# Performance work log

Hardware: AMD Instinct MI355X
Metric: run time of the kernel (lower is better)

The kernel has to match this reference:

```python
import jax, jax.numpy as jnp
import numpy as np

B, V, J, K, G, L, E = 8, 262144, 64, 4, 2048, 8, 1835008


def _qmul(q1, q2):
    # quaternion product, (w, x, y, z) convention; broadcasts over leading dims
    w1, v1 = q1[..., :1], q1[..., 1:]
    w2, v2 = q2[..., :1], q2[..., 1:]
    w = w1 * w2 - jnp.sum(v1 * v2, axis=-1, keepdims=True)
    v = w1 * v2 + w2 * v1 + jnp.cross(v1, v2)
    return jnp.concatenate([w, v], axis=-1)


def _qrot(q, v):
    # rotate vector v by unit quaternion q (w, x, y, z)
    qv, qw = q[..., 1:], q[..., :1]
    return v + 2.0 * jnp.cross(qv, jnp.cross(qv, v) + qw * v)


def setup_inputs() -> dict:
    key = jax.random.key(0)
    ks = jax.random.split(key, 13)
    return {
        "temp_verts": jax.random.normal(ks[0], (V, 3), dtype=jnp.float32),
        "joint_quat": jax.random.normal(ks[1], (B, J, 4), dtype=jnp.float32),
        "joint_trans": jax.random.normal(ks[2], (B, J, 3), dtype=jnp.float32),
        "skin_w": jax.random.uniform(ks[3], (V, K), dtype=jnp.float32),
        "node_pos": jax.random.normal(ks[4], (G, 3), dtype=jnp.float32),
        "node_quat": jax.random.normal(ks[5], (B, G, 4), dtype=jnp.float32),
        "node_trans": jax.random.normal(ks[6], (B, G, 3), dtype=jnp.float32),
        "link_w": jax.random.uniform(ks[7], (V, L), dtype=jnp.float32),
        "lap_w": jax.random.normal(ks[8], (E,), dtype=jnp.float32) * 0.1,
        "skin_idx": jax.random.randint(ks[9], (V, K), 0, J),
        "link_idx": jax.random.randint(ks[10], (V, L), 0, G),
        "lap_st": jax.random.randint(ks[11], (E,), 0, V),
        "lap_ed": jax.random.randint(ks[12], (E,), 0, V),
    }


def reference(temp_verts, joint_quat, joint_trans, skin_w, node_pos, node_quat,
              node_trans, link_w, lap_w, skin_idx, link_idx, lap_st, lap_ed):
    eps = 1e-8
    # ----- embedded-graph deformation of the template -----
    lw = link_w / (jnp.sum(link_w, axis=-1, keepdims=True) + eps)      # [V,L]
    nq = node_quat[:, link_idx]                                        # [B,V,L,4]
    nq = nq / (jnp.linalg.norm(nq, axis=-1, keepdims=True) + eps)
    nt = node_trans[:, link_idx]                                       # [B,V,L,3]
    gp = node_pos[link_idx]                                            # [V,L,3]
    local = temp_verts[:, None, :] - gp                                # [V,L,3]
    warped = _qrot(nq, local[None]) + gp[None] + nt                    # [B,V,L,3]
    v_eg = jnp.sum(lw[None, :, :, None] * warped, axis=2)              # [B,V,3]

    # ----- dual-quaternion skinning -----
    jq = joint_quat / (jnp.linalg.norm(joint_quat, axis=-1, keepdims=True) + eps)  # [B,J,4]
    t0 = jnp.concatenate([jnp.zeros_like(joint_trans[..., :1]), joint_trans], axis=-1)
    jd = 0.5 * _qmul(t0, jq)                                           # dual part [B,J,4]

    sw = skin_w / (jnp.sum(skin_w, axis=-1, keepdims=True) + eps)      # [V,K]
    r = jq[:, skin_idx]                                                # [B,V,K,4]
    d = jd[:, skin_idx]                                                # [B,V,K,4]
    # sign-fix against first influence to avoid antipodal blending
    sgn = jnp.where(jnp.sum(r * r[..., :1, :], axis=-1, keepdims=True) >= 0.0, 1.0, -1.0)
    w = sw[None, :, :, None] * sgn                                     # [B,V,K,1]
    rb = jnp.sum(w * r, axis=2)                                        # [B,V,4]
    db = jnp.sum(w * d, axis=2)                                        # [B,V,4]
    nrm = jnp.linalg.norm(rb, axis=-1, keepdims=True) + eps
    rb, db = rb / nrm, db / nrm
    rw, rv = rb[..., :1], rb[..., 1:]
    dw, dv = db[..., :1], db[..., 1:]
    trans = 2.0 * (rw * dv - dw * rv + jnp.cross(rv, dv))              # [B,V,3]
    posed = _qrot(rb, v_eg) + trans                                    # [B,V,3]

    # ----- sparse Laplacian regularization term (COO scatter) -----
    def _lap(p):
        return jax.ops.segment_sum(lap_w[:, None] * p[lap_ed], lap_st, num_segments=V)
    lap = jax.vmap(_lap)(posed)                                        # [B,V,3]

    return jnp.stack([posed, lap], axis=0)                             # [2,B,V,3]
```

## Files before the change

kernel.cpp:

```cpp
#include <hip/hip_runtime.h>
#include <hip/hip_bf16.h>
#include <math.h>

constexpr int B = 8;
constexpr int V = 262144;
constexpr int J = 64;
constexpr int K = 4;
constexpr int G = 2048;
constexpr int L = 8;
constexpr int E = 1835008;
constexpr float EPS = 1e-8f;
constexpr int PT5 = 1024;
constexpr int NB2 = 512;
constexpr int VB2 = V / NB2;
constexpr int PBLK = 256;
constexpr int EPP = E / PBLK;
constexpr int LT = 512;
constexpr int CHK = 2048;

__device__ inline unsigned bf16bits(float x) {
  unsigned u = __float_as_uint(x);
  return (u + 0x7fffu + ((u >> 16) & 1u)) >> 16;
}
__device__ inline float bflo(unsigned u) { return __uint_as_float(u << 16); }
__device__ inline float bfhi(unsigned u) {
  return __uint_as_float(u & 0xffff0000u);
}

__global__ __launch_bounds__(256) void jqd_kernel(
    const float* __restrict__ jquat, const float* __restrict__ jtrans,
    float* __restrict__ ws) {
  int i = blockIdx.x * blockDim.x + threadIdx.x;
  if (i >= B * J) return;
  float qw = jquat[i * 4 + 0];
  float qx = jquat[i * 4 + 1];
  float qy = jquat[i * 4 + 2];
  float qz = jquat[i * 4 + 3];
  float inv = 1.0f / (sqrtf(qw * qw + qx * qx + qy * qy + qz * qz) + EPS);
  qw *= inv; qx *= inv; qy *= inv; qz *= inv;
  float tx = jtrans[i * 3 + 0];
  float ty = jtrans[i * 3 + 1];
  float tz = jtrans[i * 3 + 2];
  float dw = -0.5f * (tx * qx + ty * qy + tz * qz);
  float dx = 0.5f * (qw * tx + (ty * qz - tz * qy));
  float dy = 0.5f * (qw * ty + (tz * qx - tx * qz));
  float dz = 0.5f * (qw * tz + (tx * qy - ty * qx));
  float* o = ws + (size_t)i * 8;
  o[0] = qw; o[1] = qx; o[2] = qy; o[3] = qz;
  o[4] = dw; o[5] = dx; o[6] = dy; o[7] = dz;
}

__global__ __launch_bounds__(256) void nmat_kernel(
    const float* __restrict__ npos, const float* __restrict__ nquat,
    const float* __restrict__ ntrans, float* __restrict__ nmt) {
  int i = blockIdx.x * blockDim.x + threadIdx.x;
  if (i >= B * G) return;
  int g = i & (G - 1);
  float4 q = *reinterpret_cast<const float4*>(nquat + (size_t)i * 4);
  float qw = q.x, qx = q.y, qy = q.z, qz = q.w;
  float inv = 1.0f / (sqrtf(qw * qw + qx * qx + qy * qy + qz * qz) + EPS);
  qw *= inv; qx *= inv; qy *= inv; qz *= inv;
  float xx = qx * qx, yy = qy * qy, zz = qz * qz;
  float xy = qx * qy, xz = qx * qz, yz = qy * qz;
  float wx = qw * qx, wy = qw * qy, wz = qw * qz;
  float m00 = 1.f - 2.f * (yy + zz), m01 = 2.f * (xy - wz), m02 = 2.f * (xz + wy);
  float m10 = 2.f * (xy + wz), m11 = 1.f - 2.f * (xx + zz), m12 = 2.f * (yz - wx);
  float m20 = 2.f * (xz - wy), m21 = 2.f * (yz + wx), m22 = 1.f - 2.f * (xx + yy);
  float gx = npos[g * 3 + 0], gy = npos[g * 3 + 1], gz = npos[g * 3 + 2];
  float tx = ntrans[(size_t)i * 3 + 0] + gx - (m00 * gx + m01 * gy + m02 * gz);
  float ty = ntrans[(size_t)i * 3 + 1] + gy - (m10 * gx + m11 * gy + m12 * gz);
  float tz = ntrans[(size_t)i * 3 + 2] + gz - (m20 * gx + m21 * gy + m22 * gz);
  float4* o = reinterpret_cast<float4*>(nmt + (size_t)i * 12);
  o[0] = make_float4(m00, m01, m02, tx);
  o[1] = make_float4(m10, m11, m12, ty);
  o[2] = make_float4(m20, m21, m22, tz);
}

__global__ __launch_bounds__(PT5) void posed5_kernel(
    const float* __restrict__ tv, const float* __restrict__ sw_in,
    const float* __restrict__ lw_in, const int* __restrict__ sidx,
    const int* __restrict__ lidx, const float* __restrict__ nmt,
    const float* __restrict__ jqd, float* __restrict__ out,
    unsigned* __restrict__ pvm16, int mode) {
  extern __shared__ float4 sm4[];
  int v = blockIdx.x * PT5 + threadIdx.x;

  float px = tv[(size_t)v * 3 + 0];
  float py = tv[(size_t)v * 3 + 1];
  float pz = tv[(size_t)v * 3 + 2];

  int4 si = *reinterpret_cast<const int4*>(sidx + (size_t)v * 4);
  float4 swv = *reinterpret_cast<const float4*>(sw_in + (size_t)v * 4);
  int4 li0 = *reinterpret_cast<const int4*>(lidx + (size_t)v * 8);
  int4 li1 = *reinterpret_cast<const int4*>(lidx + (size_t)v * 8 + 4);
  float4 lw0 = *reinterpret_cast<const float4*>(lw_in + (size_t)v * 8);
  float4 lw1 = *reinterpret_cast<const float4*>(lw_in + (size_t)v * 8 + 4);

  float sinv = 1.0f / (swv.x + swv.y + swv.z + swv.w + EPS);
  float swn[K] = {swv.x * sinv, swv.y * sinv, swv.z * sinv, swv.w * sinv};
  int sj[K] = {si.x, si.y, si.z, si.w};

  float linv =
      1.0f / (lw0.x + lw0.y + lw0.z + lw0.w + lw1.x + lw1.y + lw1.z + lw1.w + EPS);
  float lwn[L] = {lw0.x * linv, lw0.y * linv, lw0.z * linv, lw0.w * linv,
                  lw1.x * linv, lw1.y * linv, lw1.z * linv, lw1.w * linv};
  int gi[L] = {li0.x * 3, li0.y * 3, li0.z * 3, li0.w * 3,
               li1.x * 3, li1.y * 3, li1.z * 3, li1.w * 3};

  constexpr size_t LAPOFF = (size_t)B * V * 3;
  unsigned pk[2 * B];

  for (int b = 0; b < B; ++b) {
    __syncthreads();
    const float4* src = reinterpret_cast<const float4*>(nmt + (size_t)b * G * 12);
#pragma unroll
    for (int it = 0; it < (G * 3) / PT5; ++it) {
      int q = it * PT5 + threadIdx.x;
      sm4[q] = src[q];
    }
    __syncthreads();

    float ex = 0.f, ey = 0.f, ez = 0.f;
#pragma unroll
    for (int l = 0; l < L; ++l) {
      float4 r0 = sm4[gi[l] + 0];
      float4 r1 = sm4[gi[l] + 1];
      float4 r2 = sm4[gi[l] + 2];
      float w = lwn[l];
      ex += w * (r0.x * px + r0.y * py + r0.z * pz + r0.w);
      ey += w * (r1.x * px + r1.y * py + r1.z * pz + r1.w);
      ez += w * (r2.x * px + r2.y * py + r2.z * pz + r2.w);
    }

    float rbw = 0.f, rbx = 0.f, rby = 0.f, rbz = 0.f;
    float dbw = 0.f, dbx = 0.f, dby = 0.f, dbz = 0.f;
    float r0w = 0.f, r0x = 0.f, r0y = 0.f, r0z = 0.f;
#pragma unroll
    for (int k = 0; k < K; ++k) {
      const float* eptr = jqd + ((size_t)b * J + sj[k]) * 8;
      float4 qf = *reinterpret_cast<const float4*>(eptr);
      float4 df = *reinterpret_cast<const float4*>(eptr + 4);
      float qw = qf.x, qx = qf.y, qy = qf.z, qz = qf.w;
      if (k == 0) { r0w = qw; r0x = qx; r0y = qy; r0z = qz; }
      float dotr = qw * r0w + qx * r0x + qy * r0y + qz * r0z;
      float s = (dotr >= 0.0f) ? swn[k] : -swn[k];
      rbw += s * qw; rbx += s * qx; rby += s * qy; rbz += s * qz;
      dbw += s * df.x; dbx += s * df.y; dby += s * df.z; dbz += s * df.w;
    }
    float ninv = 1.0f / (sqrtf(rbw * rbw + rbx * rbx + rby * rby + rbz * rbz) + EPS);
    rbw *= ninv; rbx *= ninv; rby *= ninv; rbz *= ninv;
    dbw *= ninv; dbx *= ninv; dby *= ninv; dbz *= ninv;

    float txx = 2.0f * (rbw * dbx - dbw * rbx + (rby * dbz - rbz * dby));
    float tyy = 2.0f * (rbw * dby - dbw * rby + (rbz * dbx - rbx * dbz));
    float tzz = 2.0f * (rbw * dbz - dbw * rbz + (rbx * dby - rby * dbx));

    float cx = rby * ez - rbz * ey + rbw * ex;
    float cy = rbz * ex - rbx * ez + rbw * ey;
    float cz = rbx * ey - rby * ex + rbw * ez;
    float ox = ex + 2.0f * (rby * cz - rbz * cy) + txx;
    float oy = ey + 2.0f * (rbz * cx - rbx * cz) + tyy;
    float oz = ez + 2.0f * (rbx * cy - rby * cx) + tzz;

    size_t o = ((size_t)b * V + v) * 3;
    out[o + 0] = ox; out[o + 1] = oy; out[o + 2] = oz;
    pk[b * 2 + 0] = bf16bits(ox) | (bf16bits(oy) << 16);
    pk[b * 2 + 1] = bf16bits(oz);
    if (mode == 2) {
      out[LAPOFF + o + 0] = 0.f;
      out[LAPOFF + o + 1] = 0.f;
      out[LAPOFF + o + 2] = 0.f;
    }
  }

  if (mode == 0) {
    uint4* dst = reinterpret_cast<uint4*>(pvm16 + (size_t)v * 16);
    dst[0] = make_uint4(pk[0], pk[1], pk[2], pk[3]);
    dst[1] = make_uint4(pk[4], pk[5], pk[6], pk[7]);
    dst[2] = make_uint4(pk[8], pk[9], pk[10], pk[11]);
    dst[3] = make_uint4(pk[12], pk[13], pk[14], pk[15]);
  }
}

__global__ __launch_bounds__(256) void cnt512_kernel(const int* __restrict__ st,
                                                     int* __restrict__ bcnt) {
  __shared__ int h[NB2];
  int blk = blockIdx.x, t = threadIdx.x;
  h[t] = 0;
  h[t + 256] = 0;
  __syncthreads();
  int e0 = blk * EPP;
  for (int i = e0 + t; i < e0 + EPP; i += 256) atomicAdd(&h[st[i] >> 9], 1);
  __syncthreads();
  bcnt[t * PBLK + blk] = h[t];
  bcnt[(t + 256) * PBLK + blk] = h[t + 256];
}

__global__ __launch_bounds__(256) void scanA_kernel(const int* __restrict__ in,
                                                    int* __restrict__ out,
                                                    int* __restrict__ bs) {
  __shared__ int s[256];
  int t = threadIdx.x;
  int i = blockIdx.x * 256 + t;
  int x = in[i];
  s[t] = x;
  __syncthreads();
  for (int off = 1; off < 256; off <<= 1) {
    int v = (t >= off) ? s[t - off] : 0;
    __syncthreads();
    s[t] += v;
    __syncthreads();
  }
  out[i] = s[t] - x;
  if (t == 255) bs[blockIdx.x] = s[t];
}

__global__ __launch_bounds__(512) void scanB_kernel(int* __restrict__ bs) {
  __shared__ int s[NB2];
  int t = threadIdx.x;
  int x = bs[t];
  s[t] = x;
  __syncthreads();
  for (int off = 1; off < NB2; off <<= 1) {
    int v = (t >= off) ? s[t - off] : 0;
    __syncthreads();
    s[t] += v;
    __syncthreads();
  }
  bs[t] = s[t] - x;
}

__global__ __launch_bounds__(256) void scanC_kernel(int* __restrict__ out,
                                                    const int* __restrict__ bs) {
  out[blockIdx.x * 256 + threadIdx.x] += bs[blockIdx.x];
}

__global__ __launch_bounds__(256) void part512_kernel(
    const int* __restrict__ st, const int* __restrict__ ed,
    const float* __restrict__ w, const int* __restrict__ boff2,
    int2* __restrict__ ewB) {
  __shared__ int lbase[NB2];
  __shared__ int lcur[NB2];
  int blk = blockIdx.x, t = threadIdx.x;
  lbase[t] = boff2[t * PBLK + blk];
  lbase[t + 256] = boff2[(t + 256) * PBLK + blk];
  lcur[t] = 0;
  lcur[t + 256] = 0;
  __syncthreads();
  int e0 = blk * EPP;
  for (int i = e0 + t; i < e0 + EPP; i += 256) {
    int s = st[i];
    int b = s >> 9;
    int pos = lbase[b] + atomicAdd(&lcur[b], 1);
    ewB[pos] = make_int2(((s & 511) << 18) | ed[i], __float_as_int(w[i]));
  }
}

__global__ __launch_bounds__(LT, 8) void lap_sorted_kernel(
    const int2* __restrict__ ewB, const int* __restrict__ boff2,
    const unsigned* __restrict__ pvm16, float* __restrict__ lap) {
  __shared__ int2 eL[CHK];
  __shared__ int rs[VB2];
  __shared__ int cur[VB2];
  __shared__ int wsum[8];
  int p = blockIdx.x, t = threadIdx.x;
  int lane = t & 63, wid = t >> 6;
  int beg = boff2[p * PBLK];
  int end = (p < NB2 - 1) ? boff2[(p + 1) * PBLK] : E;

  float acc[24];
#pragma unroll
  for (int i = 0; i < 24; ++i) acc[i] = 0.f;

  for (int cbeg = beg; cbeg < end; cbeg += CHK) {
    int cnt = min(CHK, end - cbeg);
    rs[t] = 0;
    __syncthreads();

    int2 er[CHK / LT];
#pragma unroll
    for (int j = 0; j < CHK / LT; ++j) {
      int idx = j * LT + t;
      if (idx < cnt) {
        er[j] = ewB[cbeg + idx];
        atomicAdd(&rs[((unsigned)er[j].x) >> 18], 1);
      }
    }
    __syncthreads();

    int x = rs[t];
    int incl = x;
#pragma unroll
    for (int off = 1; off < 64; off <<= 1) {
      int y = __shfl_up(incl, off, 64);
      if (lane >= off) incl += y;
    }
    if (lane == 63) wsum[wid] = incl;
    __syncthreads();
    if (t < 8) {
      int s = wsum[t];
#pragma unroll
      for (int off = 1; off < 8; off <<= 1) {
        int y = __shfl_up(s, off, 64);
        if (t >= off) s += y;
      }
      wsum[t] = s;
    }
    __syncthreads();
    int wbase = (wid == 0) ? 0 : wsum[wid - 1];
    int excl = incl + wbase - x;
    __syncthreads();
    rs[t] = excl;
    cur[t] = excl;
    __syncthreads();

#pragma unroll
    for (int j = 0; j < CHK / LT; ++j) {
      int idx = j * LT + t;
      if (idx < cnt) {
        int sl = ((unsigned)er[j].x) >> 18;
        int pos = atomicAdd(&cur[sl], 1);
        eL[pos] = er[j];
      }
    }
    __syncthreads();

    int rbeg = rs[t];
    int rend = (t < VB2 - 1) ? rs[t + 1] : cnt;
    for (int j = rbeg; j < rend; ++j) {
      int2 ew = eL[j];
      float w = __int_as_float(ew.y);
      int d = ew.x & 0x3ffff;
      const uint4* q = reinterpret_cast<const uint4*>(pvm16 + (size_t)d * 16);
      uint4 q0 = q[0], q1 = q[1], q2 = q[2], q3 = q[3];
      unsigned u[16] = {q0.x, q0.y, q0.z, q0.w, q1.x, q1.y, q1.z, q1.w,
                        q2.x, q2.y, q2.z, q2.w, q3.x, q3.y, q3.z, q3.w};
#pragma unroll
      for (int b = 0; b < B; ++b) {
        acc[b * 3 + 0] += w * bflo(u[2 * b]);
        acc[b * 3 + 1] += w * bfhi(u[2 * b]);
        acc[b * 3 + 2] += w * bflo(u[2 * b + 1]);
      }
    }
    __syncthreads();
  }

  int v = p * VB2 + t;
#pragma unroll
  for (int b = 0; b < B; ++b) {
    size_t o = ((size_t)b * V + v) * 3;
    lap[o + 0] = acc[b * 3 + 0];
    lap[o + 1] = acc[b * 3 + 1];
    lap[o + 2] = acc[b * 3 + 2];
  }
}

__global__ __launch_bounds__(256) void lap_atomic_kernel(
    const float* __restrict__ lapw, const int* __restrict__ st,
    const int* __restrict__ ed, const float* __restrict__ posed,
    float* __restrict__ lap) {
  int e = blockIdx.x * blockDim.x + threadIdx.x;
  if (e >= E) return;
  float w = lapw[e];
  int s = st[e];
  int d = ed[e];
#pragma unroll
  for (int b = 0; b < B; ++b) {
    size_t pb = ((size_t)b * V + d) * 3;
    size_t ob = ((size_t)b * V + s) * 3;
    atomicAdd(&lap[ob + 0], w * posed[pb + 0]);
    atomicAdd(&lap[ob + 1], w * posed[pb + 1]);
    atomicAdd(&lap[ob + 2], w * posed[pb + 2]);
  }
}

extern "C" void kernel_launch(void* const* d_in, const int* in_sizes, int n_in,
                              void* d_out, int out_size, void* d_ws, size_t ws_size,
                              hipStream_t stream) {
  const float* tv    = (const float*)d_in[0];
  const float* jquat = (const float*)d_in[1];
  const float* jtran = (const float*)d_in[2];
  const float* sw    = (const float*)d_in[3];
  const float* npos  = (const float*)d_in[4];
  const float* nquat = (const float*)d_in[5];
  const float* ntran = (const float*)d_in[6];
  const float* lw    = (const float*)d_in[7];
  const float* lapw  = (const float*)d_in[8];
  const int*   sidx  = (const int*)d_in[9];
  const int*   lidx  = (const int*)d_in[10];
  const int*   lst   = (const int*)d_in[11];
  const int*   led   = (const int*)d_in[12];
  float* out = (float*)d_out;
  float* lap = out + (size_t)B * V * 3;

  float*    jqd   = (float*)d_ws;
  float*    nmt   = jqd + 4096;
  int*      bcnt  = (int*)(nmt + (size_t)B * G * 12);
  int*      boff2 = bcnt + NB2 * PBLK;
  int*      bsum  = boff2 + NB2 * PBLK;
  int2*     ewB   = (int2*)(bsum + NB2 + 60);
  unsigned* pvm16 = (unsigned*)(ewB + E);
  size_t need = (size_t)((char*)(pvm16 + (size_t)V * 16) - (char*)d_ws);
  int tier = (ws_size >= need) ? 0 : 2;

  jqd_kernel<<<(B * J + 255) / 256, 256, 0, stream>>>(jquat, jtran, jqd);
  nmat_kernel<<<(B * G + 255) / 256, 256, 0, stream>>>(npos, nquat, ntran, nmt);

  if (tier == 0) {
    cnt512_kernel<<<PBLK, 256, 0, stream>>>(lst, bcnt);
    scanA_kernel<<<NB2, 256, 0, stream>>>(bcnt, boff2, bsum);
    scanB_kernel<<<1, NB2, 0, stream>>>(bsum);
    scanC_kernel<<<NB2, 256, 0, stream>>>(boff2, bsum);
    part512_kernel<<<PBLK, 256, 0, stream>>>(lst, led, lapw, boff2, ewB);
    posed5_kernel<<<V / PT5, PT5, G * 3 * sizeof(float4), stream>>>(
        tv, sw, lw, sidx, lidx, nmt, jqd, out, pvm16, 0);
    lap_sorted_kernel<<<NB2, LT, 0, stream>>>(ewB, boff2, pvm16, lap);
  } else {
    posed5_kernel<<<V / PT5, PT5, G * 3 * sizeof(float4), stream>>>(
        tv, sw, lw, sidx, lidx, nmt, jqd, out, (unsigned*)jqd , 2);
    lap_atomic_kernel<<<E / 256, 256, 0, stream>>>(lapw, lst, led, out, lap);
  }
}
```

Before: 175.8 us.

## Stage joint dual quaternions in LDS and split Laplacian rows across two half-blocks

The joint dual-quaternion table is stored as separate q and d float4 arrays and copied into shared memory once per posing block, so the per-vertex skinning gathers read LDS instead of global memory. The sorted Laplacian kernel now runs 1024 threads per block. Two threads process alternating edges of each destination row, and the two partial sums are combined through shared memory. This is meant to raise occupancy and memory-level parallelism in the gather-heavy Laplacian pass, at the cost of extra LDS use and a final reduction step.

```diff
diff --git a/kernel.cpp b/kernel.cpp
--- a/kernel.cpp
+++ b/kernel.cpp
@@ -15,8 +15,8 @@
 constexpr int VB2 = V / NB2;
 constexpr int PBLK = 256;
 constexpr int EPP = E / PBLK;
-constexpr int LT = 512;
 constexpr int CHK = 2048;
+constexpr int JQO = G * 3;
 
 __device__ inline unsigned bf16bits(float x) {
   unsigned u = __float_as_uint(x);
@@ -45,9 +45,10 @@
   float dx = 0.5f * (qw * tx + (ty * qz - tz * qy));
   float dy = 0.5f * (qw * ty + (tz * qx - tx * qz));
   float dz = 0.5f * (qw * tz + (tx * qy - ty * qx));
-  float* o = ws + (size_t)i * 8;
-  o[0] = qw; o[1] = qx; o[2] = qy; o[3] = qz;
-  o[4] = dw; o[5] = dx; o[6] = dy; o[7] = dz;
+  float4* qfp = reinterpret_cast<float4*>(ws);
+  float4* dfp = qfp + B * J;
+  qfp[i] = make_float4(qw, qx, qy, qz);
+  dfp[i] = make_float4(dw, dx, dy, dz);
 }
 
 __global__ __launch_bounds__(256) void nmat_kernel(
@@ -76,14 +77,17 @@
   o[2] = make_float4(m20, m21, m22, tz);
 }
 
-__global__ __launch_bounds__(PT5) void posed5_kernel(
+__global__ __launch_bounds__(PT5) void posed5b_kernel(
     const float* __restrict__ tv, const float* __restrict__ sw_in,
     const float* __restrict__ lw_in, const int* __restrict__ sidx,
     const int* __restrict__ lidx, const float* __restrict__ nmt,
     const float* __restrict__ jqd, float* __restrict__ out,
     unsigned* __restrict__ pvm16, int mode) {
   extern __shared__ float4 sm4[];
-  int v = blockIdx.x * PT5 + threadIdx.x;
+  int t = threadIdx.x;
+  int v = blockIdx.x * PT5 + t;
+
+  sm4[JQO + t] = reinterpret_cast<const float4*>(jqd)[t];
 
   float px = tv[(size_t)v * 3 + 0];
   float py = tv[(size_t)v * 3 + 1];
@@ -115,7 +119,7 @@
     const float4* src = reinterpret_cast<const float4*>(nmt + (size_t)b * G * 12);
 #pragma unroll
     for (int it = 0; it < (G * 3) / PT5; ++it) {
-      int q = it * PT5 + threadIdx.x;
+      int q = it * PT5 + t;
       sm4[q] = src[q];
     }
     __syncthreads();
@@ -137,9 +141,8 @@
     float r0w = 0.f, r0x = 0.f, r0y = 0.f, r0z = 0.f;
 #pragma unroll
     for (int k = 0; k < K; ++k) {
-      const float* eptr = jqd + ((size_t)b * J + sj[k]) * 8;
-      float4 qf = *reinterpret_cast<const float4*>(eptr);
-      float4 df = *reinterpret_cast<const float4*>(eptr + 4);
+      float4 qf = sm4[JQO + (b << 6) + sj[k]];
+      float4 df = sm4[JQO + 512 + (b << 6) + sj[k]];
       float qw = qf.x, qx = qf.y, qy = qf.z, qz = qf.w;
       if (k == 0) { r0w = qw; r0x = qx; r0y = qy; r0z = qz; }
       float dotr = qw * r0w + qx * r0x + qy * r0y + qz * r0z;
@@ -256,15 +259,18 @@
   }
 }
 
-__global__ __launch_bounds__(LT, 8) void lap_sorted_kernel(
+__global__ __launch_bounds__(1024, 8) void lap_sorted2_kernel(
     const int2* __restrict__ ewB, const int* __restrict__ boff2,
     const unsigned* __restrict__ pvm16, float* __restrict__ lap) {
-  __shared__ int2 eL[CHK];
-  __shared__ int rs[VB2];
-  __shared__ int cur[VB2];
-  __shared__ int wsum[8];
+  extern __shared__ char smraw[];
+  int2* eL = reinterpret_cast<int2*>(smraw);
+  float* accF = reinterpret_cast<float*>(smraw);
+  int* rs = reinterpret_cast<int*>(smraw + 49152);
+  int* cur = rs + NB2 / 1;
+  int* wsum = cur + 512;
   int p = blockIdx.x, t = threadIdx.x;
   int lane = t & 63, wid = t >> 6;
+  int vt = t & 511, half = t >> 9;
   int beg = boff2[p * PBLK];
   int end = (p < NB2 - 1) ? boff2[(p + 1) * PBLK] : E;
 
@@ -274,13 +280,13 @@
 
   for (int cbeg = beg; cbeg < end; cbeg += CHK) {
     int cnt = min(CHK, end - cbeg);
-    rs[t] = 0;
-    __syncthreads();
-
-    int2 er[CHK / LT];
-#pragma unroll
-    for (int j = 0; j < CHK / LT; ++j) {
-      int idx = j * LT + t;
+    if (t < 512) rs[t] = 0;
+    __syncthreads();
+
+    int2 er[CHK / 1024];
+#pragma unroll
+    for (int j = 0; j < CHK / 1024; ++j) {
+      int idx = j * 1024 + t;
       if (idx < cnt) {
         er[j] = ewB[cbeg + idx];
         atomicAdd(&rs[((unsigned)er[j].x) >> 18], 1);
@@ -288,14 +294,17 @@
     }
     __syncthreads();
 
-    int x = rs[t];
-    int incl = x;
-#pragma unroll
-    for (int off = 1; off < 64; off <<= 1) {
-      int y = __shfl_up(incl, off, 64);
-      if (lane >= off) incl += y;
-    }
-    if (lane == 63) wsum[wid] = incl;
+    int x = 0, incl = 0;
+    if (t < 512) {
+      x = rs[t];
+      incl = x;
+#pragma unroll
+      for (int off = 1; off < 64; off <<= 1) {
+        int y = __shfl_up(incl, off, 64);
+        if (lane >= off) incl += y;
+      }
+      if (lane == 63) wsum[wid] = incl;
+    }
     __syncthreads();
     if (t < 8) {
       int s = wsum[t];
@@ -307,16 +316,17 @@
       wsum[t] = s;
     }
     __syncthreads();
-    int wbase = (wid == 0) ? 0 : wsum[wid - 1];
-    int excl = incl + wbase - x;
-    __syncthreads();
-    rs[t] = excl;
-    cur[t] = excl;
-    __syncthreads();
-
-#pragma unroll
-    for (int j = 0; j < CHK / LT; ++j) {
-      int idx = j * LT + t;
+    if (t < 512) {
+      int wbase = (wid == 0) ? 0 : wsum[wid - 1];
+      int excl = incl + wbase - x;
+      rs[t] = excl;
+      cur[t] = excl;
+    }
+    __syncthreads();
+
+#pragma unroll
+    for (int j = 0; j < CHK / 1024; ++j) {
+      int idx = j * 1024 + t;
       if (idx < cnt) {
         int sl = ((unsigned)er[j].x) >> 18;
         int pos = atomicAdd(&cur[sl], 1);
@@ -325,9 +335,9 @@
     }
     __syncthreads();
 
-    int rbeg = rs[t];
-    int rend = (t < VB2 - 1) ? rs[t + 1] : cnt;
-    for (int j = rbeg; j < rend; ++j) {
+    int rbeg = rs[vt];
+    int rend = (vt < 511) ? rs[vt + 1] : cnt;
+    for (int j = rbeg + half; j < rend; j += 2) {
       int2 ew = eL[j];
       float w = __int_as_float(ew.y);
       int d = ew.x & 0x3ffff;
@@ -345,13 +355,20 @@
     __syncthreads();
   }
 
-  int v = p * VB2 + t;
-#pragma unroll
-  for (int b = 0; b < B; ++b) {
-    size_t o = ((size_t)b * V + v) * 3;
-    lap[o + 0] = acc[b * 3 + 0];
-    lap[o + 1] = acc[b * 3 + 1];
-    lap[o + 2] = acc[b * 3 + 2];
+  if (half == 1) {
+#pragma unroll
+    for (int i = 0; i < 24; ++i) accF[vt * 24 + i] = acc[i];
+  }
+  __syncthreads();
+  if (half == 0) {
+    int v = p * VB2 + vt;
+#pragma unroll
+    for (int b = 0; b < B; ++b) {
+      size_t o = ((size_t)b * V + v) * 3;
+      lap[o + 0] = acc[b * 3 + 0] + accF[vt * 24 + b * 3 + 0];
+      lap[o + 1] = acc[b * 3 + 1] + accF[vt * 24 + b * 3 + 1];
+      lap[o + 2] = acc[b * 3 + 2] + accF[vt * 24 + b * 3 + 2];
+    }
   }
 }
 
@@ -403,6 +420,9 @@
   size_t need = (size_t)((char*)(pvm16 + (size_t)V * 16) - (char*)d_ws);
   int tier = (ws_size >= need) ? 0 : 2;
 
+  constexpr size_t POSED_LDS = (size_t)(G * 3 + 1024) * sizeof(float4);
+  constexpr size_t LAP_LDS = 49152 + (512 + 512 + 16) * sizeof(int);
+
   jqd_kernel<<<(B * J + 255) / 256, 256, 0, stream>>>(jquat, jtran, jqd);
   nmat_kernel<<<(B * G + 255) / 256, 256, 0, stream>>>(npos, nquat, ntran, nmt);
 
@@ -412,11 +432,11 @@
     scanB_kernel<<<1, NB2, 0, stream>>>(bsum);
     scanC_kernel<<<NB2, 256, 0, stream>>>(boff2, bsum);
     part512_kernel<<<PBLK, 256, 0, stream>>>(lst, led, lapw, boff2, ewB);
-    posed5_kernel<<<V / PT5, PT5, G * 3 * sizeof(float4), stream>>>(
+    posed5b_kernel<<<V / PT5, PT5, POSED_LDS, stream>>>(
         tv, sw, lw, sidx, lidx, nmt, jqd, out, pvm16, 0);
-    lap_sorted_kernel<<<NB2, LT, 0, stream>>>(ewB, boff2, pvm16, lap);
+    lap_sorted2_kernel<<<NB2, 1024, LAP_LDS, stream>>>(ewB, boff2, pvm16, lap);
   } else {
-    posed5_kernel<<<V / PT5, PT5, G * 3 * sizeof(float4), stream>>>(
+    posed5b_kernel<<<V / PT5, PT5, POSED_LDS, stream>>>(
         tv, sw, lw, sidx, lidx, nmt, jqd, out, (unsigned*)jqd , 2);
     lap_atomic_kernel<<<E / 256, 256, 0, stream>>>(lapw, lst, led, out, lap);
   }
```

After: 158.5 us. 1.11x faster.
